# Optimization experiments

Measured on AMD Instinct MI355X. Metric: run time of the kernel, lower is better.

## Reference

```python
import jax, jax.numpy as jnp
import numpy as np

ANGSTROM_TO_METER = 1e-10
COULOMB_CONSTANT = 8987551792.3
ELECTRON_CHARGE = 1.602176634e-19
EV_TO_JOULE = 1.602176634e-19
COUL_DAMPING_BETA = 18.7
R0_METER = 2.2 * ANGSTROM_TO_METER
EWALD_P = 0.3275911
EWALD_A = (0.254829592, -0.284496736, 1.421413741, -1.453152027, 1.061405429)
EWALD_F = 2.0

N_ATOMS = 200000
N_EDGES = 8000000
N_GRAPHS = 256


def setup_inputs() -> dict:
    key = jax.random.key(0)
    k1, k2, k3, k4, k5 = jax.random.split(key, 5)
    dij = jax.random.normal(k1, (N_EDGES, 3), dtype=jnp.float32)  # Angstrom
    pred_charge = jax.random.normal(k2, (N_ATOMS,), dtype=jnp.float32)  # e
    g_ewald = jnp.full((1,), 3.0e9, dtype=jnp.float32)  # 1/m (~0.3 1/A)
    row = jax.random.randint(k3, (N_EDGES,), 0, N_ATOMS)
    col = jax.random.randint(k4, (N_EDGES,), 0, N_ATOMS)
    batch = jnp.sort(jax.random.randint(k5, (N_ATOMS,), 0, N_GRAPHS))
    return {"dij": dij, "pred_charge": pred_charge, "g_ewald": g_ewald,
            "row": row, "col": col, "batch": batch}


def reference(dij, pred_charge, g_ewald, row, col, batch):
    n_atoms = pred_charge.shape[0]
    dij_m = dij * ANGSTROM_TO_METER                      # [E,3] meters
    rij = jnp.sqrt(jnp.sum(dij_m * dij_m, axis=-1))      # [E]
    q = pred_charge * ELECTRON_CHARGE                    # Coulombs
    prefactor = COULOMB_CONSTANT * q[row] * q[col] / rij
    # exponential short-range damping below r0
    damp = jnp.where(rij < R0_METER,
                     jnp.exp(-COUL_DAMPING_BETA * (R0_METER - rij) / R0_METER),
                     jnp.ones_like(rij))
    ecoul = 0.5 * prefactor * damp
    fcoul = prefactor * damp / rij
    # Ewald real-space correction via Abramowitz-Stegun erfc polynomial
    grij = g_ewald[0] * rij
    expm2 = jnp.exp(-grij * grij)
    t = 1.0 / (1.0 + EWALD_P * grij)
    a0, a1, a2, a3, a4 = EWALD_A
    erfc = t * (a0 + t * (a1 + t * (a2 + t * (a3 + t * a4)))) * expm2
    ecoul = ecoul + prefactor * (erfc - 1.0)
    fcoul = fcoul + prefactor * (erfc + EWALD_F * grij * expm2 - 1.0) / rij
    # per-edge force vector, converted J/m -> eV/A
    fij = dij_m * (fcoul / rij)[:, None]                 # [E,3]
    fij_ev = fij * ANGSTROM_TO_METER / EV_TO_JOULE
    ecoul_ev = ecoul / EV_TO_JOULE
    # scatter edge->atom (by row), then atom->molecule (by batch)
    e_atom = jax.ops.segment_sum(ecoul_ev, row, num_segments=n_atoms)
    coul_energy = jax.ops.segment_sum(e_atom, batch, num_segments=N_GRAPHS)
    force_row = jax.ops.segment_sum(fij_ev, row, num_segments=n_atoms)
    force_col = jax.ops.segment_sum(fij_ev, col, num_segments=n_atoms)
    coul_force = force_row - force_col
    return coul_energy, coul_force
```

## Files before the change

### kernel.cpp

```cpp
#include <hip/hip_runtime.h>
#include <hip/hip_fp16.h>

#define N_GRAPHS_C 256
#define CHUNK_LOG 12
#define CHUNK (1 << CHUNK_LOG)
#define MAXB 64
#define NSLICE 12
#define NSLICE_FB 10
#define TPA 256
#define TPBB 512
#define FP_SCALE 1024.0f
#define FP_INV   (1.0f / 1024.0f)

__device__ __forceinline__ void edge_math(
    float dx, float dy, float dz, float qr, float qc, float gA,
    float& fx, float& fy, float& fz, float& ecoul)
{
    const float KEV = (float)(8987551792.3 * 1.602176634e-9);
    float r2 = dx * dx + dy * dy + dz * dz;
    float inv_r = rsqrtf(r2);
    float rA = r2 * inv_r;

    float pref = KEV * qr * qc * inv_r;

    float damp = 1.0f;
    if (rA < 2.2f)
        damp = __expf(-18.7f * (2.2f - rA) * (1.0f / 2.2f));

    float grij = gA * rA;
    float expm2 = __expf(-grij * grij);
    float t = 1.0f / (1.0f + 0.3275911f * grij);
    float erfc = t * (0.254829592f +
                 t * (-0.284496736f +
                 t * (1.421413741f +
                 t * (-1.453152027f +
                 t * 1.061405429f)))) * expm2;

    ecoul = pref * (0.5f * damp + (erfc - 1.0f));
    float S = damp + erfc + 2.0f * grij * expm2 - 1.0f;
    float fs = pref * S * (inv_r * inv_r);
    fx = dx * fs; fy = dy * fs; fz = dz * fs;
}

__device__ __forceinline__ uint2 pack_rec(float fx, float fy, float fz, unsigned lid)
{
    uint2 u;
    u.x = __builtin_bit_cast(unsigned, __floats2half2_rn(fx, fy));
    u.y = (__builtin_bit_cast(unsigned, __floats2half2_rn(fz, 0.0f)) & 0xFFFFu) |
          (lid << 16);
    return u;
}

__device__ __forceinline__ void acc_rec(int* acc, unsigned w0, unsigned w1)
{
    float2 xy = __half22float2(__builtin_bit_cast(__half2, w0));
    float fz = __half2float(__builtin_bit_cast(__half2, w1).x);
    unsigned idx = w1 >> 16;
    atomicAdd(&acc[idx],             __float2int_rn(xy.x * FP_SCALE));
    atomicAdd(&acc[CHUNK + idx],     __float2int_rn(xy.y * FP_SCALE));
    atomicAdd(&acc[2 * CHUNK + idx], __float2int_rn(fz   * FP_SCALE));
}

__global__ __launch_bounds__(256) void prep_qg(
    const float* __restrict__ q, const int* __restrict__ batch,
    float2* __restrict__ qg, float* __restrict__ ovf, int n_atoms)
{
    int i = blockIdx.x * 256 + threadIdx.x;
    if (i < n_atoms) {
        qg[i] = make_float2(q[i], __int_as_float(batch[i]));
        ovf[3 * i + 0] = 0.f;
        ovf[3 * i + 1] = 0.f;
        ovf[3 * i + 2] = 0.f;
    }
}

__global__ __launch_bounds__(TPA) void passA(
    const float* __restrict__ dij, const float2* __restrict__ qg,
    const float* __restrict__ g_ewald,
    const int* __restrict__ row, const int* __restrict__ col,
    uint2* __restrict__ records, int cap,
    unsigned* __restrict__ cnt_table,
    float* __restrict__ e_part,
    float* __restrict__ ovf,
    int n_edges, int nb, int tile_g)
{
    __shared__ unsigned cnt[MAXB];
    __shared__ float e_graph[4 * N_GRAPHS_C];

    int tid = threadIdx.x;
    if (tid < MAXB) cnt[tid] = 0u;
    for (int i = tid; i < 4 * N_GRAPHS_C; i += TPA) e_graph[i] = 0.f;
    __syncthreads();

    float* e_my = &e_graph[(tid >> 6) * N_GRAPHS_C];

    int n4 = n_edges >> 2;
    int g0 = blockIdx.x * tile_g;
    int g1 = min(g0 + tile_g, n4);

    const int4* row4 = (const int4*)row;
    const int4* col4 = (const int4*)col;
    const float4* dij4 = (const float4*)dij;

    const float gA = g_ewald[0] * 1e-10f;
    size_t blk_base = (size_t)blockIdx.x * nb * cap;

    int g = g0 + tid;
    int4 r_cur = make_int4(0, 0, 0, 0), c_cur = make_int4(0, 0, 0, 0);
    int4 r_nxt = make_int4(0, 0, 0, 0), c_nxt = make_int4(0, 0, 0, 0);
    float2 vr_cur[4], vc_cur[4];

    if (g < g1) {
        r_cur = row4[g]; c_cur = col4[g];
        vr_cur[0] = qg[r_cur.x]; vc_cur[0] = qg[c_cur.x];
        vr_cur[1] = qg[r_cur.y]; vc_cur[1] = qg[c_cur.y];
        vr_cur[2] = qg[r_cur.z]; vc_cur[2] = qg[c_cur.z];
        vr_cur[3] = qg[r_cur.w]; vc_cur[3] = qg[c_cur.w];
    }
    if (g + TPA < g1) { r_nxt = row4[g + TPA]; c_nxt = col4[g + TPA]; }

    while (g < g1) {
        int gn = g + TPA;

        float2 vr_n[4], vc_n[4];
        vr_n[0] = qg[r_nxt.x]; vc_n[0] = qg[c_nxt.x];
        vr_n[1] = qg[r_nxt.y]; vc_n[1] = qg[c_nxt.y];
        vr_n[2] = qg[r_nxt.z]; vc_n[2] = qg[c_nxt.z];
        vr_n[3] = qg[r_nxt.w]; vc_n[3] = qg[c_nxt.w];

        int4 r_n2 = make_int4(0, 0, 0, 0), c_n2 = make_int4(0, 0, 0, 0);
        if (gn + TPA < g1) { r_n2 = row4[gn + TPA]; c_n2 = col4[gn + TPA]; }

        float4 d0 = dij4[3 * g + 0];
        float4 d1 = dij4[3 * g + 1];
        float4 d2 = dij4[3 * g + 2];
        float ex[4] = {d0.x, d0.w, d1.z, d2.y};
        float ey[4] = {d0.y, d1.x, d1.w, d2.z};
        float ez[4] = {d0.z, d1.y, d2.x, d2.w};
        int rr[4] = {r_cur.x, r_cur.y, r_cur.z, r_cur.w};
        int cc[4] = {c_cur.x, c_cur.y, c_cur.z, c_cur.w};

        #pragma unroll
        for (int j = 0; j < 4; ++j) {
            int r = rr[j], c = cc[j];
            float fx, fy, fz, ec;
            edge_math(ex[j], ey[j], ez[j], vr_cur[j].x, vc_cur[j].x, gA,
                      fx, fy, fz, ec);

            atomicAdd(&e_my[__float_as_int(vr_cur[j].y)], ec);

            int br = r >> CHUNK_LOG, bc = c >> CHUNK_LOG;
            unsigned pr = atomicAdd(&cnt[br], 1u);
            unsigned pc = atomicAdd(&cnt[bc], 1u);
            if (pr < (unsigned)cap)
                records[blk_base + (size_t)br * cap + pr] =
                    pack_rec(fx, fy, fz, (unsigned)(r & (CHUNK - 1)));
            else {
                atomicAdd(&ovf[3 * r + 0], fx);
                atomicAdd(&ovf[3 * r + 1], fy);
                atomicAdd(&ovf[3 * r + 2], fz);
            }
            if (pc < (unsigned)cap)
                records[blk_base + (size_t)bc * cap + pc] =
                    pack_rec(-fx, -fy, -fz, (unsigned)(c & (CHUNK - 1)));
            else {
                atomicAdd(&ovf[3 * c + 0], -fx);
                atomicAdd(&ovf[3 * c + 1], -fy);
                atomicAdd(&ovf[3 * c + 2], -fz);
            }
        }

        g = gn;
        r_cur = r_nxt; c_cur = c_nxt;
        r_nxt = r_n2;  c_nxt = c_n2;
        #pragma unroll
        for (int j = 0; j < 4; ++j) { vr_cur[j] = vr_n[j]; vc_cur[j] = vc_n[j]; }
    }
    __syncthreads();

    if (tid < nb) cnt_table[(size_t)blockIdx.x * nb + tid] = min(cnt[tid], (unsigned)cap);
    for (int g2 = tid; g2 < N_GRAPHS_C; g2 += TPA)
        e_part[(size_t)blockIdx.x * N_GRAPHS_C + g2] =
            e_graph[g2] + e_graph[N_GRAPHS_C + g2] +
            e_graph[2 * N_GRAPHS_C + g2] + e_graph[3 * N_GRAPHS_C + g2];
}

__global__ __launch_bounds__(TPBB) void passB(
    const uint2* __restrict__ records, int cap,
    const unsigned* __restrict__ cnt_table,
    int* __restrict__ partial, int nblkA, int nb, int nslice)
{
    __shared__ int acc[3 * CHUNK];

    int b = blockIdx.x / nslice;
    int s = blockIdx.x % nslice;
    int k0 = (int)((long long)s * nblkA / nslice);
    int k1 = (int)((long long)(s + 1) * nblkA / nslice);

    for (int i = threadIdx.x; i < 3 * CHUNK; i += TPBB) acc[i] = 0;
    __syncthreads();

    int wid  = threadIdx.x >> 6;
    int lane = threadIdx.x & 63;

    for (int k = k0 + wid; k < k1; k += TPBB / 64) {
        unsigned n = cnt_table[(size_t)k * nb + b];
        const uint2* rec = records + ((size_t)k * nb + b) * cap;
        const uint4* rec4 = (const uint4*)rec;
        unsigned nh = n >> 1;
        for (unsigned i = lane; i < nh; i += 64) {
            uint4 v = rec4[i];
            acc_rec(acc, v.x, v.y);
            acc_rec(acc, v.z, v.w);
        }
        if ((n & 1u) && lane == 0) {
            uint2 t = rec[n - 1];
            acc_rec(acc, t.x, t.y);
        }
    }
    __syncthreads();

    int* dst = partial + (size_t)blockIdx.x * 3 * CHUNK;
    for (int i = threadIdx.x; i < 3 * CHUNK; i += TPBB) dst[i] = acc[i];
}

__global__ __launch_bounds__(256) void fin_force(
    const int* __restrict__ partial, const float* __restrict__ ovf,
    const float* __restrict__ e_part,
    float* __restrict__ force, float* __restrict__ energy,
    int n_atoms, int nslice, int nblkA, int nfblk)
{
    if ((int)blockIdx.x >= nfblk) {
        int g = (blockIdx.x - nfblk) * 4 + (threadIdx.x >> 6);
        int lane = threadIdx.x & 63;
        float s = 0.f;
        for (int k = lane; k < nblkA; k += 64)
            s += e_part[(size_t)k * N_GRAPHS_C + g];
        for (int off = 32; off > 0; off >>= 1) s += __shfl_down(s, off, 64);
        if (lane == 0) energy[g] = s;
        return;
    }
    int a = blockIdx.x * 256 + threadIdx.x;
    if (a >= n_atoms) return;
    int b = a >> CHUNK_LOG, l = a & (CHUNK - 1);
    long long sx = 0, sy = 0, sz = 0;
    const int* p = partial + (size_t)b * nslice * 3 * CHUNK + l;
    for (int s = 0; s < nslice; ++s) {
        const int* ps = p + (size_t)s * 3 * CHUNK;
        sx += ps[0]; sy += ps[CHUNK]; sz += ps[2 * CHUNK];
    }
    force[3 * a + 0] = ovf[3 * a + 0] + (float)sx * FP_INV;
    force[3 * a + 1] = ovf[3 * a + 1] + (float)sy * FP_INV;
    force[3 * a + 2] = ovf[3 * a + 2] + (float)sz * FP_INV;
}

__global__ __launch_bounds__(1024) void chunk_kernel(
    const float* __restrict__ dij, const float* __restrict__ q,
    const float* __restrict__ g_ewald,
    const int* __restrict__ row, const int* __restrict__ col,
    float* __restrict__ partial, int n_edges, int n_chunks, int n_slices)
{
    __shared__ float acc[CHUNK * 4];
    int c = blockIdx.x % n_chunks;
    int p = blockIdx.x / n_chunks;
    int cbase = c << CHUNK_LOG;
    for (int i = threadIdx.x; i < CHUNK * 4; i += 1024) acc[i] = 0.f;
    __syncthreads();
    const float gA = g_ewald[0] * 1e-10f;
    int n4 = (n_edges + 3) >> 2;
    int g0 = (int)((long long)p * n4 / n_slices);
    int g1 = (int)((long long)(p + 1) * n4 / n_slices);
    const int4* row4 = (const int4*)row;
    const int4* col4 = (const int4*)col;
    for (int g = g0 + threadIdx.x; g < g1; g += 1024) {
        int4 r4 = row4[g];
        int4 c4 = col4[g];
        int rr[4] = {r4.x, r4.y, r4.z, r4.w};
        int cc[4] = {c4.x, c4.y, c4.z, c4.w};
        #pragma unroll
        for (int j = 0; j < 4; ++j) {
            int e = 4 * g + j;
            if (e >= n_edges) break;
            int rl = rr[j] - cbase;
            int cl = cc[j] - cbase;
            bool hr = (unsigned)rl < (unsigned)CHUNK;
            bool hc = (unsigned)cl < (unsigned)CHUNK;
            if (!(hr || hc)) continue;
            float fx, fy, fz, ec;
            edge_math(dij[3 * e], dij[3 * e + 1], dij[3 * e + 2],
                      q[rr[j]], q[cc[j]], gA, fx, fy, fz, ec);
            if (hr) {
                atomicAdd(&acc[4 * rl + 0], fx);
                atomicAdd(&acc[4 * rl + 1], fy);
                atomicAdd(&acc[4 * rl + 2], fz);
                atomicAdd(&acc[4 * rl + 3], ec);
            }
            if (hc) {
                atomicAdd(&acc[4 * cl + 0], -fx);
                atomicAdd(&acc[4 * cl + 1], -fy);
                atomicAdd(&acc[4 * cl + 2], -fz);
            }
        }
    }
    __syncthreads();
    float4* dst = (float4*)partial + (size_t)(c * n_slices + p) * CHUNK;
    const float4* src = (const float4*)acc;
    for (int i = threadIdx.x; i < CHUNK; i += 1024) dst[i] = src[i];
}

__global__ __launch_bounds__(256) void finalize_kernel(
    const float* __restrict__ partial, const int* __restrict__ batch,
    float* __restrict__ energy, float* __restrict__ force,
    int n_atoms, int n_slices)
{
    int i = blockIdx.x * blockDim.x + threadIdx.x;
    float fx = 0.f, fy = 0.f, fz = 0.f, en = 0.f;
    if (i < n_atoms) {
        int c = i >> CHUNK_LOG;
        int l = i & (CHUNK - 1);
        const float4* base = (const float4*)partial + (size_t)c * n_slices * CHUNK + l;
        for (int p = 0; p < n_slices; ++p) {
            float4 v = base[(size_t)p * CHUNK];
            fx += v.x; fy += v.y; fz += v.z; en += v.w;
        }
        force[3 * i + 0] = fx;
        force[3 * i + 1] = fy;
        force[3 * i + 2] = fz;
    }
    int ic = i < n_atoms ? i : (n_atoms - 1);
    int b = batch[ic];
    float v = (i < n_atoms) ? en : 0.0f;
    int b0 = __shfl(b, 0, 64);
    unsigned long long m = __ballot(b == b0);
    if (m == ~0ull) {
        for (int off = 32; off > 0; off >>= 1)
            v += __shfl_down(v, off, 64);
        if ((threadIdx.x & 63) == 0) atomicAdd(&energy[b0], v);
    } else {
        atomicAdd(&energy[b], v);
    }
}

extern "C" void kernel_launch(void* const* d_in, const int* in_sizes, int n_in,
                              void* d_out, int out_size, void* d_ws, size_t ws_size,
                              hipStream_t stream) {
    const float* dij     = (const float*)d_in[0];
    const float* q       = (const float*)d_in[1];
    const float* g_ewald = (const float*)d_in[2];
    const int*   row     = (const int*)d_in[3];
    const int*   col     = (const int*)d_in[4];
    const int*   batch   = (const int*)d_in[5];

    int n_edges = in_sizes[0] / 3;
    int n_atoms = in_sizes[1];

    float* energy = (float*)d_out;
    float* force  = (float*)d_out + N_GRAPHS_C;

    int nb = (n_atoms + CHUNK - 1) >> CHUNK_LOG;
    int n4 = n_edges >> 2;

    size_t sz_partial = (size_t)nb * NSLICE * 3 * CHUNK * sizeof(int);
    size_t sz_ovf     = (size_t)3 * n_atoms * sizeof(float);
    size_t sz_qg      = (size_t)n_atoms * sizeof(float2);

    const int  tile_sel[2]   = {1024, 2048};
    const int  mincap_sel[2] = {224, 416};
    const int  capmax_sel[2] = {256, 512};

    int tile_g = 0, cap = 0, nblkA = 0;
    size_t sz_epart = 0, sz_cnt = 0;
    for (int t = 0; t < 2 && tile_g == 0; ++t) {
        int nba = (n4 + tile_sel[t] - 1) / tile_sel[t];
        size_t se = (size_t)nba * N_GRAPHS_C * sizeof(float);
        size_t sc = (size_t)nba * nb * sizeof(unsigned);
        size_t fixed = ((sz_partial + 255) & ~(size_t)255) +
                       ((se         + 255) & ~(size_t)255) +
                       ((sc         + 255) & ~(size_t)255) +
                       ((sz_ovf     + 255) & ~(size_t)255) +
                       ((sz_qg      + 255) & ~(size_t)255) + 512;
        if ((long long)ws_size > (long long)fixed) {
            long long c = ((long long)ws_size - (long long)fixed) /
                          ((long long)nba * nb * 8);
            c = (c / 32) * 32;
            if (c > capmax_sel[t]) c = capmax_sel[t];
            if (c >= mincap_sel[t]) {
                tile_g = tile_sel[t]; cap = (int)c; nblkA = nba;
                sz_epart = se; sz_cnt = sc;
            }
        }
    }

    bool fast = (nb <= MAXB) && ((n_edges & 3) == 0) && (tile_g > 0);

    if (fast) {
        char* ws = (char*)d_ws;
        size_t off = 0;
        uint2*    records  = (uint2*)(ws + off);
        off += (size_t)nblkA * nb * cap * 8;   off = (off + 255) & ~(size_t)255;
        int*      partial  = (int*)(ws + off);
        off += sz_partial;                     off = (off + 255) & ~(size_t)255;
        float*    e_part   = (float*)(ws + off);
        off += sz_epart;                       off = (off + 255) & ~(size_t)255;
        unsigned* cnt_tab  = (unsigned*)(ws + off);
        off += sz_cnt;                         off = (off + 255) & ~(size_t)255;
        float*    ovf      = (float*)(ws + off);
        off += sz_ovf;                         off = (off + 255) & ~(size_t)255;
        float2*   qg       = (float2*)(ws + off);

        prep_qg<<<(n_atoms + 255) / 256, 256, 0, stream>>>(q, batch, qg, ovf, n_atoms);

        passA<<<nblkA, TPA, 0, stream>>>(
            dij, qg, g_ewald, row, col,
            records, cap, cnt_tab, e_part, ovf, n_edges, nb, tile_g);

        passB<<<nb * NSLICE, TPBB, 0, stream>>>(
            records, cap, cnt_tab, partial, nblkA, nb, NSLICE);

        int nfblk = (n_atoms + 255) / 256;
        fin_force<<<nfblk + N_GRAPHS_C / 4, 256, 0, stream>>>(
            partial, ovf, e_part, force, energy, n_atoms, NSLICE, nblkA, nfblk);
    } else {
        size_t need_chunk = (size_t)nb * NSLICE_FB * CHUNK * 4 * sizeof(float);
        if (ws_size >= need_chunk) {
            hipMemsetAsync(d_out, 0, N_GRAPHS_C * sizeof(float), stream);
            chunk_kernel<<<nb * NSLICE_FB, 1024, 0, stream>>>(
                dij, q, g_ewald, row, col, (float*)d_ws, n_edges, nb, NSLICE_FB);
            finalize_kernel<<<(n_atoms + 255) / 256, 256, 0, stream>>>(
                (const float*)d_ws, batch, energy, force, n_atoms, NSLICE_FB);
        }
    }
}
```

Measured before the change: 397.0 us.

## Stage per-bucket force records in LDS and flush them coalesced per phase

passA now writes packed force records into a shared-memory staging buffer per atom bucket (64 slots each), then after each 256-thread phase every wavefront flushes whole buckets to global records with one atomic reservation and contiguous lane writes. This replaces scattered per-edge global stores with coalesced bursts and reduces global counter contention. In exchange it adds two block barriers per phase and about 32KB of LDS, which can lower occupancy, and staging overflow falls back to global atomics. The fast path now also requires tile_g to be a multiple of the block size.

```diff
diff --git a/kernel.cpp b/kernel.cpp
--- a/kernel.cpp
+++ b/kernel.cpp
@@ -9,6 +9,7 @@
 #define NSLICE_FB 10
 #define TPA 256
 #define TPBB 512
+#define SD 64
 #define FP_SCALE 1024.0f
 #define FP_INV   (1.0f / 1024.0f)
 
@@ -84,19 +85,24 @@
     float* __restrict__ ovf,
     int n_edges, int nb, int tile_g)
 {
+    __shared__ uint2    stage[MAXB][SD];
+    __shared__ unsigned scnt[MAXB];
     __shared__ unsigned cnt[MAXB];
-    __shared__ float e_graph[4 * N_GRAPHS_C];
-
-    int tid = threadIdx.x;
-    if (tid < MAXB) cnt[tid] = 0u;
+    __shared__ float    e_graph[4 * N_GRAPHS_C];
+
+    int tid  = threadIdx.x;
+    int wid  = tid >> 6;
+    int lane = tid & 63;
+    if (tid < MAXB) { scnt[tid] = 0u; cnt[tid] = 0u; }
     for (int i = tid; i < 4 * N_GRAPHS_C; i += TPA) e_graph[i] = 0.f;
     __syncthreads();
 
-    float* e_my = &e_graph[(tid >> 6) * N_GRAPHS_C];
+    float* e_my = &e_graph[wid * N_GRAPHS_C];
 
     int n4 = n_edges >> 2;
-    int g0 = blockIdx.x * tile_g;
-    int g1 = min(g0 + tile_g, n4);
+    int gbase = blockIdx.x * tile_g;
+    int g1 = min(gbase + tile_g, n4);
+    int nph = tile_g / TPA;
 
     const int4* row4 = (const int4*)row;
     const int4* col4 = (const int4*)col;
@@ -105,22 +111,63 @@
     const float gA = g_ewald[0] * 1e-10f;
     size_t blk_base = (size_t)blockIdx.x * nb * cap;
 
-    int g = g0 + tid;
     int4 r_cur = make_int4(0, 0, 0, 0), c_cur = make_int4(0, 0, 0, 0);
-    int4 r_nxt = make_int4(0, 0, 0, 0), c_nxt = make_int4(0, 0, 0, 0);
     float2 vr_cur[4], vc_cur[4];
-
-    if (g < g1) {
-        r_cur = row4[g]; c_cur = col4[g];
+    {
+        int g = gbase + tid;
+        if (g < g1) { r_cur = row4[g]; c_cur = col4[g]; }
         vr_cur[0] = qg[r_cur.x]; vc_cur[0] = qg[c_cur.x];
         vr_cur[1] = qg[r_cur.y]; vc_cur[1] = qg[c_cur.y];
         vr_cur[2] = qg[r_cur.z]; vc_cur[2] = qg[c_cur.z];
         vr_cur[3] = qg[r_cur.w]; vc_cur[3] = qg[c_cur.w];
     }
-    if (g + TPA < g1) { r_nxt = row4[g + TPA]; c_nxt = col4[g + TPA]; }
-
-    while (g < g1) {
-        int gn = g + TPA;
+
+    for (int p = 0; p < nph; ++p) {
+        int g = gbase + p * TPA + tid;
+
+        int4 r_nxt = make_int4(0, 0, 0, 0), c_nxt = make_int4(0, 0, 0, 0);
+        if (p + 1 < nph && g + TPA < g1) {
+            r_nxt = row4[g + TPA]; c_nxt = col4[g + TPA];
+        }
+
+        if (g < g1) {
+            float4 d0 = dij4[3 * g + 0];
+            float4 d1 = dij4[3 * g + 1];
+            float4 d2 = dij4[3 * g + 2];
+            float ex[4] = {d0.x, d0.w, d1.z, d2.y};
+            float ey[4] = {d0.y, d1.x, d1.w, d2.z};
+            float ez[4] = {d0.z, d1.y, d2.x, d2.w};
+            int rr[4] = {r_cur.x, r_cur.y, r_cur.z, r_cur.w};
+            int cc[4] = {c_cur.x, c_cur.y, c_cur.z, c_cur.w};
+
+            #pragma unroll
+            for (int j = 0; j < 4; ++j) {
+                int r = rr[j], c = cc[j];
+                float fx, fy, fz, ec;
+                edge_math(ex[j], ey[j], ez[j], vr_cur[j].x, vc_cur[j].x, gA,
+                          fx, fy, fz, ec);
+
+                atomicAdd(&e_my[__float_as_int(vr_cur[j].y)], ec);
+
+                int br = r >> CHUNK_LOG, bc = c >> CHUNK_LOG;
+                unsigned pr = atomicAdd(&scnt[br], 1u);
+                unsigned pc = atomicAdd(&scnt[bc], 1u);
+                if (pr < SD)
+                    stage[br][pr] = pack_rec(fx, fy, fz, (unsigned)(r & (CHUNK - 1)));
+                else {
+                    atomicAdd(&ovf[3 * r + 0], fx);
+                    atomicAdd(&ovf[3 * r + 1], fy);
+                    atomicAdd(&ovf[3 * r + 2], fz);
+                }
+                if (pc < SD)
+                    stage[bc][pc] = pack_rec(-fx, -fy, -fz, (unsigned)(c & (CHUNK - 1)));
+                else {
+                    atomicAdd(&ovf[3 * c + 0], -fx);
+                    atomicAdd(&ovf[3 * c + 1], -fy);
+                    atomicAdd(&ovf[3 * c + 2], -fz);
+                }
+            }
+        }
 
         float2 vr_n[4], vc_n[4];
         vr_n[0] = qg[r_nxt.x]; vc_n[0] = qg[c_nxt.x];
@@ -128,55 +175,35 @@
         vr_n[2] = qg[r_nxt.z]; vc_n[2] = qg[c_nxt.z];
         vr_n[3] = qg[r_nxt.w]; vc_n[3] = qg[c_nxt.w];
 
-        int4 r_n2 = make_int4(0, 0, 0, 0), c_n2 = make_int4(0, 0, 0, 0);
-        if (gn + TPA < g1) { r_n2 = row4[gn + TPA]; c_n2 = col4[gn + TPA]; }
-
-        float4 d0 = dij4[3 * g + 0];
-        float4 d1 = dij4[3 * g + 1];
-        float4 d2 = dij4[3 * g + 2];
-        float ex[4] = {d0.x, d0.w, d1.z, d2.y};
-        float ey[4] = {d0.y, d1.x, d1.w, d2.z};
-        float ez[4] = {d0.z, d1.y, d2.x, d2.w};
-        int rr[4] = {r_cur.x, r_cur.y, r_cur.z, r_cur.w};
-        int cc[4] = {c_cur.x, c_cur.y, c_cur.z, c_cur.w};
-
-        #pragma unroll
-        for (int j = 0; j < 4; ++j) {
-            int r = rr[j], c = cc[j];
-            float fx, fy, fz, ec;
-            edge_math(ex[j], ey[j], ez[j], vr_cur[j].x, vc_cur[j].x, gA,
-                      fx, fy, fz, ec);
-
-            atomicAdd(&e_my[__float_as_int(vr_cur[j].y)], ec);
-
-            int br = r >> CHUNK_LOG, bc = c >> CHUNK_LOG;
-            unsigned pr = atomicAdd(&cnt[br], 1u);
-            unsigned pc = atomicAdd(&cnt[bc], 1u);
-            if (pr < (unsigned)cap)
-                records[blk_base + (size_t)br * cap + pr] =
-                    pack_rec(fx, fy, fz, (unsigned)(r & (CHUNK - 1)));
-            else {
-                atomicAdd(&ovf[3 * r + 0], fx);
-                atomicAdd(&ovf[3 * r + 1], fy);
-                atomicAdd(&ovf[3 * r + 2], fz);
+        __syncthreads();
+
+        for (int b = wid; b < nb; b += TPA / 64) {
+            unsigned m = min(scnt[b], (unsigned)SD);
+            unsigned base = 0;
+            if (lane == 0) base = atomicAdd(&cnt[b], m);
+            base = (unsigned)__shfl((int)base, 0, 64);
+            for (unsigned i = lane; i < m; i += 64) {
+                uint2 rv = stage[b][i];
+                unsigned slot = base + i;
+                if (slot < (unsigned)cap) {
+                    records[blk_base + (size_t)b * cap + slot] = rv;
+                } else {
+                    float2 xy = __half22float2(__builtin_bit_cast(__half2, rv.x));
+                    float fzv = __half2float(__builtin_bit_cast(__half2, rv.y).x);
+                    int atom = (b << CHUNK_LOG) + (int)(rv.y >> 16);
+                    atomicAdd(&ovf[3 * atom + 0], xy.x);
+                    atomicAdd(&ovf[3 * atom + 1], xy.y);
+                    atomicAdd(&ovf[3 * atom + 2], fzv);
+                }
             }
-            if (pc < (unsigned)cap)
-                records[blk_base + (size_t)bc * cap + pc] =
-                    pack_rec(-fx, -fy, -fz, (unsigned)(c & (CHUNK - 1)));
-            else {
-                atomicAdd(&ovf[3 * c + 0], -fx);
-                atomicAdd(&ovf[3 * c + 1], -fy);
-                atomicAdd(&ovf[3 * c + 2], -fz);
-            }
-        }
-
-        g = gn;
+            if (lane == 0) scnt[b] = 0u;
+        }
+        __syncthreads();
+
         r_cur = r_nxt; c_cur = c_nxt;
-        r_nxt = r_n2;  c_nxt = c_n2;
         #pragma unroll
         for (int j = 0; j < 4; ++j) { vr_cur[j] = vr_n[j]; vc_cur[j] = vc_n[j]; }
     }
-    __syncthreads();
 
     if (tid < nb) cnt_table[(size_t)blockIdx.x * nb + tid] = min(cnt[tid], (unsigned)cap);
     for (int g2 = tid; g2 < N_GRAPHS_C; g2 += TPA)
@@ -391,7 +418,8 @@
         }
     }
 
-    bool fast = (nb <= MAXB) && ((n_edges & 3) == 0) && (tile_g > 0);
+    bool fast = (nb <= MAXB) && ((n_edges & 3) == 0) && (tile_g > 0) &&
+                ((tile_g % TPA) == 0);
 
     if (fast) {
         char* ws = (char*)d_ws;
```

Result: faster. 360.2 us (-9.3%).
